# Kernel optimization log

Hardware: AMD Instinct MI355X
Metric: run time of the kernel (lower is better)

## Reference

```python
import jax, jax.numpy as jnp
import numpy as np

B, L, D, H, FF = 2, 4096, 512, 8, 2048
HD = D // H
EPS = 1e-5


def _layer_norm(x, g, b):
    mu = jnp.mean(x, axis=-1, keepdims=True)
    var = jnp.mean(jnp.square(x - mu), axis=-1, keepdims=True)
    return (x - mu) * jax.lax.rsqrt(var + EPS) * g + b


def setup_inputs() -> dict:
    key = jax.random.key(0)
    ks = jax.random.split(key, 16)
    s = 1.0 / np.sqrt(D)
    inp = {
        'x': jax.random.normal(ks[0], (B, L, D), dtype=jnp.float32),
        'Wq': jax.random.normal(ks[1], (D, D), dtype=jnp.float32) * s,
        'bq': jnp.zeros((D,), jnp.float32),
        'Wk': jax.random.normal(ks[2], (D, D), dtype=jnp.float32) * s,
        'bk': jnp.zeros((D,), jnp.float32),
        'Wv': jax.random.normal(ks[3], (D, D), dtype=jnp.float32) * s,
        'bv': jnp.zeros((D,), jnp.float32),
        'Wo': jax.random.normal(ks[4], (D, D), dtype=jnp.float32) * s,
        'bo': jnp.zeros((D,), jnp.float32),
        'ln1_g': jnp.ones((D,), jnp.float32),
        'ln1_b': jnp.zeros((D,), jnp.float32),
        'W1': jax.random.normal(ks[5], (D, FF), dtype=jnp.float32) * s,
        'b1': jnp.zeros((FF,), jnp.float32),
        'W2': jax.random.normal(ks[6], (FF, D), dtype=jnp.float32) * (1.0 / np.sqrt(FF)),
        'b2': jnp.zeros((D,), jnp.float32),
        'ln2_g': jnp.ones((D,), jnp.float32),
        'ln2_b': jnp.zeros((D,), jnp.float32),
        'window': 128,
    }
    return inp


def reference(x, Wq, bq, Wk, bk, Wv, bv, Wo, bo, ln1_g, ln1_b, W1, b1, W2, b2, ln2_g, ln2_b, window):
    # ---- local (banded) self-attention, matching nn.MultiheadAttention math ----
    q = (x @ Wq + bq).reshape(B, L, H, HD)
    k = (x @ Wk + bk).reshape(B, L, H, HD)
    v = (x @ Wv + bv).reshape(B, L, H, HD)
    scale = 1.0 / np.sqrt(HD)
    scores = jnp.einsum('bqhd,bkhd->bhqk', q, k) * scale  # [B,H,L,L]
    idx = jnp.arange(L)
    band = jnp.abs(idx[None, :] - idx[:, None]) > window   # True = masked
    scores = jnp.where(band[None, None], -jnp.inf, scores)
    probs = jax.nn.softmax(scores, axis=-1)
    attn = jnp.einsum('bhqk,bkhd->bqhd', probs, v).reshape(B, L, D)
    attn = attn @ Wo + bo
    # ---- residual + norm1 ----
    h = _layer_norm(x + attn, ln1_g, ln1_b)
    # ---- FFN + residual + norm2 (dropout=0 at eval) ----
    ff = jax.nn.relu(h @ W1 + b1) @ W2 + b2
    return _layer_norm(h + ff, ln2_g, ln2_b)
```

## Files before the change

kernel.cpp:

```cpp
#include <hip/hip_runtime.h>

namespace {

constexpr int B = 2, L = 4096, D = 512, H = 8, FF = 2048;
constexpr int M = B * L;
constexpr float LN_EPS = 1e-5f;

typedef __attribute__((ext_vector_type(8))) short short8;
typedef __attribute__((ext_vector_type(4))) float floatx4;

typedef __attribute__((address_space(3))) unsigned int lds_uint;
typedef const __attribute__((address_space(1))) unsigned int glob_uint;

__device__ __forceinline__ void gl_lds16(const unsigned short* g, unsigned short* l) {
  __builtin_amdgcn_global_load_lds((glob_uint*)g, (lds_uint*)l, 16, 0, 0);
}

__device__ __forceinline__ unsigned short f2bf(float f) {
  union { float f; unsigned u; } v; v.f = f;
  unsigned r = v.u + 0x7FFFu + ((v.u >> 16) & 1u);
  return (unsigned short)(r >> 16);
}

__global__ void k_prep(const float* __restrict__ x,
                       const float* __restrict__ Wq, const float* __restrict__ Wk,
                       const float* __restrict__ Wv, const float* __restrict__ Wo,
                       const float* __restrict__ W1, const float* __restrict__ W2,
                       const float* __restrict__ bq, const float* __restrict__ bk,
                       const float* __restrict__ bv,
                       unsigned short* __restrict__ Xb,
                       unsigned short* __restrict__ WqkvT,
                       unsigned short* __restrict__ WoT,
                       unsigned short* __restrict__ W1T,
                       unsigned short* __restrict__ W2T,
                       float* __restrict__ bqkv) {
  int tid = blockIdx.x * blockDim.x + threadIdx.x;
  if (tid < 1048576) {
    float4 v = ((const float4*)x)[tid];
    ushort4 o = make_ushort4(f2bf(v.x), f2bf(v.y), f2bf(v.z), f2bf(v.w));
    ((ushort4*)Xb)[tid] = o;
    return;
  }
  int u = tid - 1048576;
  if (u < 786432) {
    const float* src = (u < 262144) ? Wq : (u < 524288 ? Wk : Wv);
    int uu = u & 262143;
    int n = uu >> 9, k = uu & 511;
    WqkvT[u] = f2bf(src[k * 512 + n]);
    return;
  }
  u -= 786432;
  if (u < 262144) { int n = u >> 9, k = u & 511; WoT[u] = f2bf(Wo[k * 512 + n]); return; }
  u -= 262144;
  if (u < 1048576) { int n = u >> 9, k = u & 511; W1T[u] = f2bf(W1[k * 2048 + n]); return; }
  u -= 1048576;
  if (u < 1048576) { int n = u >> 11, k = u & 2047; W2T[u] = f2bf(W2[k * 512 + n]); return; }
  u -= 1048576;
  if (u < 1536) bqkv[u] = (u < 512) ? bq[u] : (u < 1024 ? bk[u - 512] : bv[u - 1024]);
}

template <int EPI>
__global__ __launch_bounds__(256, 3)
void k_gemm(const unsigned short* __restrict__ A, const unsigned short* __restrict__ BT,
            const float* __restrict__ bias, void* __restrict__ Cout,
            const int klen, const int N) {
  __shared__ unsigned short lA[128 * 32];
  __shared__ unsigned short lB[128 * 32];
  const int tid = threadIdx.x;
  const int wave = tid >> 6, lane = tid & 63;
  const int quad = lane >> 4, l16 = lane & 15;
  const int m0 = blockIdx.y * 128, n0 = blockIdx.x * 128;
  const int wm = (wave >> 1) * 64, wn = (wave & 1) * 64;
  const int kbeg = blockIdx.z * klen;
  const size_t Kdim = (size_t)klen * gridDim.z;

  const floatx4 fzero = {0.f, 0.f, 0.f, 0.f};
  floatx4 acc[4][4];
#pragma unroll
  for (int i = 0; i < 4; ++i)
#pragma unroll
    for (int j = 0; j < 4; ++j) acc[i][j] = fzero;

  const int r0 = tid >> 2, o0 = (tid & 3) * 8;
  const int r1 = (256 + tid) >> 2, o1 = (tid & 3) * 8;
  const unsigned short* Ag0 = A + (size_t)(m0 + r0) * Kdim + kbeg + o0;
  const unsigned short* Ag1 = A + (size_t)(m0 + r1) * Kdim + kbeg + o1;
  const unsigned short* Bg0 = BT + (size_t)(n0 + r0) * Kdim + kbeg + o0;
  const unsigned short* Bg1 = BT + (size_t)(n0 + r1) * Kdim + kbeg + o1;
  unsigned short* lA0 = &lA[wave * 512];
  unsigned short* lA1 = &lA[(4 + wave) * 512];
  unsigned short* lB0 = &lB[wave * 512];
  unsigned short* lB1 = &lB[(4 + wave) * 512];

  for (int kt = 0; kt < klen; kt += 32) {
    __syncthreads();
    gl_lds16(Ag0 + kt, lA0);
    gl_lds16(Ag1 + kt, lA1);
    gl_lds16(Bg0 + kt, lB0);
    gl_lds16(Bg1 + kt, lB1);
    __syncthreads();
    short8 af[4], bf[4];
#pragma unroll
    for (int i = 0; i < 4; ++i) af[i] = *(const short8*)&lA[(wm + i * 16 + l16) * 32 + quad * 8];
#pragma unroll
    for (int j = 0; j < 4; ++j) bf[j] = *(const short8*)&lB[(wn + j * 16 + l16) * 32 + quad * 8];
#pragma unroll
    for (int i = 0; i < 4; ++i)
#pragma unroll
      for (int j = 0; j < 4; ++j)
        acc[i][j] = __builtin_amdgcn_mfma_f32_16x16x32_bf16(af[i], bf[j], acc[i][j], 0, 0, 0);
  }

  float* outf = (float*)Cout + (size_t)blockIdx.z * M * N;
#pragma unroll
  for (int j = 0; j < 4; ++j) {
    const int col = n0 + wn + j * 16 + l16;
    const float bv = (blockIdx.z == 0) ? bias[col] : 0.f;
#pragma unroll
    for (int i = 0; i < 4; ++i) {
      const int row = m0 + wm + i * 16 + quad * 4;
#pragma unroll
      for (int r = 0; r < 4; ++r) {
        float v = acc[i][j][r] + bv;
        if (EPI == 1) v = fmaxf(v, 0.f);
        if (EPI == 2)
          outf[(size_t)(row + r) * N + col] = v;
        else
          ((unsigned short*)Cout)[(size_t)(row + r) * N + col] = f2bf(v);
      }
    }
  }
}

__global__ __launch_bounds__(256, 3)
void k_attn(const unsigned short* __restrict__ QKV, unsigned short* __restrict__ attnb,
            const int* __restrict__ wptr) {
  const int W = wptr[0];
  constexpr int VS = 324;
  __shared__ unsigned short Vt[64 * VS];
  __shared__ unsigned short Pb[4][16 * 72];
  const int tid = threadIdx.x;
  const int wave = tid >> 6, lane = tid & 63;
  const int quad = lane >> 4, l16 = lane & 15;
  const int blk = blockIdx.x;
  const int h = blk & 7, b = (blk >> 3) & 1, qt = blk >> 4;
  const int q0blk = qt * 64;
  const int q0 = q0blk + wave * 16;
  const float scale = 0.125f;

  const unsigned short* Kbase = QKV + (size_t)(b * L) * 1536 + 512 + h * 64;
  const unsigned short* Vbase = QKV + (size_t)(b * L) * 1536 + 1024 + h * 64;

#pragma unroll
  for (int i = 0; i < 10; ++i) {
    int c = tid + i * 256;
    int row = c >> 3, cd = (c & 7) * 8;
    int key = q0blk - 128 + row;
    int keyc = key < 0 ? 0 : (key > L - 1 ? L - 1 : key);
    short8 v = *(const short8*)(Vbase + (size_t)keyc * 1536 + cd);
#pragma unroll
    for (int e = 0; e < 8; ++e) Vt[(cd + e) * VS + row] = (unsigned short)v[e];
  }

  const unsigned short* Qp = QKV + (size_t)(b * L + q0 + l16) * 1536 + h * 64;
  short8 qf0 = *(const short8*)(Qp + quad * 8);
  short8 qf1 = *(const short8*)(Qp + 32 + quad * 8);

  const floatx4 fzero = {0.f, 0.f, 0.f, 0.f};
  floatx4 o[4];
#pragma unroll
  for (int i = 0; i < 4; ++i) o[i] = fzero;
  float lsum[4] = {0.f, 0.f, 0.f, 0.f};
  unsigned short* lp = Pb[wave];

  __syncthreads();

  for (int it = 0; it < 5; ++it) {
    const int jbg = q0blk - 128 + it * 64;
    floatx4 s[4];
#pragma unroll
    for (int ct = 0; ct < 4; ++ct) {
      int key = jbg + ct * 16 + l16;
      int keyc = key < 0 ? 0 : (key > L - 1 ? L - 1 : key);
      const unsigned short* Kr = Kbase + (size_t)keyc * 1536;
      floatx4 z = fzero;
      z = __builtin_amdgcn_mfma_f32_16x16x32_bf16(qf0, *(const short8*)(Kr + quad * 8), z, 0, 0, 0);
      z = __builtin_amdgcn_mfma_f32_16x16x32_bf16(qf1, *(const short8*)(Kr + 32 + quad * 8), z, 0, 0, 0);
      s[ct] = z;
    }
#pragma unroll
    for (int r = 0; r < 4; ++r) {
      int q = q0 + quad * 4 + r;
#pragma unroll
      for (int ct = 0; ct < 4; ++ct) {
        int key = jbg + ct * 16 + l16;
        int d = q - key; d = d < 0 ? -d : d;
        bool ok = (key >= 0) && (key < L) && (d <= W);
        float p = ok ? __expf(s[ct][r] * scale) : 0.f;
        lsum[r] += p;
        lp[(quad * 4 + r) * 72 + ct * 16 + l16] = f2bf(p);
      }
    }
    short8 pf0 = *(const short8*)&lp[l16 * 72 + quad * 8];
    short8 pf1 = *(const short8*)&lp[l16 * 72 + 32 + quad * 8];
#pragma unroll
    for (int nt = 0; nt < 4; ++nt) {
      const unsigned short* vp = &Vt[(nt * 16 + l16) * VS + it * 64 + quad * 8];
      o[nt] = __builtin_amdgcn_mfma_f32_16x16x32_bf16(pf0, *(const short8*)vp, o[nt], 0, 0, 0);
      o[nt] = __builtin_amdgcn_mfma_f32_16x16x32_bf16(pf1, *(const short8*)(vp + 32), o[nt], 0, 0, 0);
    }
  }
#pragma unroll
  for (int r = 0; r < 4; ++r) {
#pragma unroll
    for (int dd = 1; dd < 16; dd <<= 1) lsum[r] += __shfl_xor(lsum[r], dd, 64);
  }
#pragma unroll
  for (int r = 0; r < 4; ++r) {
    float inv = 1.f / lsum[r];
    size_t base = (size_t)(b * L + q0 + quad * 4 + r) * 512 + h * 64;
#pragma unroll
    for (int nt = 0; nt < 4; ++nt)
      attnb[base + nt * 16 + l16] = f2bf(o[nt][r] * inv);
  }
}

template <int NP>
__global__ __launch_bounds__(256, 2)
void k_res_ln(const float* __restrict__ t0, const float* __restrict__ t1,
              const float* __restrict__ res,
              const float* __restrict__ gamma, const float* __restrict__ beta,
              float* __restrict__ outf, unsigned short* __restrict__ outb) {
  const int wave = threadIdx.x >> 6, lane = threadIdx.x & 63;
  const int row = blockIdx.x * 4 + wave;
  const float4* tv = (const float4*)(t0 + (size_t)row * D);
  const float4* rv = (const float4*)(res + (size_t)row * D);
  float4 a0 = tv[lane], a1 = tv[lane + 64];
  float4 b0 = rv[lane], b1 = rv[lane + 64];
  float4 y0 = make_float4(a0.x + b0.x, a0.y + b0.y, a0.z + b0.z, a0.w + b0.w);
  float4 y1 = make_float4(a1.x + b1.x, a1.y + b1.y, a1.z + b1.z, a1.w + b1.w);
  if (NP == 2) {
    const float4* uv = (const float4*)(t1 + (size_t)row * D);
    float4 c0 = uv[lane], c1 = uv[lane + 64];
    y0.x += c0.x; y0.y += c0.y; y0.z += c0.z; y0.w += c0.w;
    y1.x += c1.x; y1.y += c1.y; y1.z += c1.z; y1.w += c1.w;
  }
  float s = y0.x + y0.y + y0.z + y0.w + y1.x + y1.y + y1.z + y1.w;
  float q = y0.x * y0.x + y0.y * y0.y + y0.z * y0.z + y0.w * y0.w +
            y1.x * y1.x + y1.y * y1.y + y1.z * y1.z + y1.w * y1.w;
#pragma unroll
  for (int d = 1; d < 64; d <<= 1) {
    s += __shfl_xor(s, d, 64);
    q += __shfl_xor(q, d, 64);
  }
  const float mean = s * (1.f / D);
  const float var = q * (1.f / D) - mean * mean;
  const float rstd = rsqrtf(var + LN_EPS);
  float4 g0 = ((const float4*)gamma)[lane], g1 = ((const float4*)gamma)[lane + 64];
  float4 e0 = ((const float4*)beta)[lane], e1 = ((const float4*)beta)[lane + 64];
  float4 o0 = make_float4((y0.x - mean) * rstd * g0.x + e0.x, (y0.y - mean) * rstd * g0.y + e0.y,
                          (y0.z - mean) * rstd * g0.z + e0.z, (y0.w - mean) * rstd * g0.w + e0.w);
  float4 o1 = make_float4((y1.x - mean) * rstd * g1.x + e1.x, (y1.y - mean) * rstd * g1.y + e1.y,
                          (y1.z - mean) * rstd * g1.z + e1.z, (y1.w - mean) * rstd * g1.w + e1.w);
  ((float4*)(outf + (size_t)row * D))[lane] = o0;
  ((float4*)(outf + (size_t)row * D))[lane + 64] = o1;
  if (outb) {
    ((ushort4*)(outb + (size_t)row * D))[lane] =
        make_ushort4(f2bf(o0.x), f2bf(o0.y), f2bf(o0.z), f2bf(o0.w));
    ((ushort4*)(outb + (size_t)row * D))[lane + 64] =
        make_ushort4(f2bf(o1.x), f2bf(o1.y), f2bf(o1.z), f2bf(o1.w));
  }
}

}

extern "C" void kernel_launch(void* const* d_in, const int* in_sizes, int n_in,
                              void* d_out, int out_size, void* d_ws, size_t ws_size,
                              hipStream_t stream) {
  const float* x   = (const float*)d_in[0];
  const float* Wq  = (const float*)d_in[1];
  const float* bq  = (const float*)d_in[2];
  const float* Wk  = (const float*)d_in[3];
  const float* bk  = (const float*)d_in[4];
  const float* Wv  = (const float*)d_in[5];
  const float* bv  = (const float*)d_in[6];
  const float* Wo  = (const float*)d_in[7];
  const float* bo  = (const float*)d_in[8];
  const float* g1  = (const float*)d_in[9];
  const float* be1 = (const float*)d_in[10];
  const float* W1  = (const float*)d_in[11];
  const float* b1  = (const float*)d_in[12];
  const float* W2  = (const float*)d_in[13];
  const float* b2  = (const float*)d_in[14];
  const float* g2  = (const float*)d_in[15];
  const float* be2 = (const float*)d_in[16];
  const int* wptr  = (const int*)d_in[17];
  float* out = (float*)d_out;

  char* w = (char*)d_ws;
  size_t off = 0;
  auto take = [&](size_t bytes) -> void* {
    void* p = w + off;
    off += (bytes + 255) & ~(size_t)255;
    return p;
  };
  unsigned short* Xb    = (unsigned short*)take((size_t)M * D * 2);
  unsigned short* QKVb  = (unsigned short*)take((size_t)M * 1536 * 2);
  unsigned short* attnb = (unsigned short*)take((size_t)M * D * 2);
  unsigned short* WqkvT = (unsigned short*)take((size_t)1536 * 512 * 2);
  unsigned short* WoT   = (unsigned short*)take((size_t)512 * 512 * 2);
  unsigned short* W1T   = (unsigned short*)take((size_t)2048 * 512 * 2);
  unsigned short* W2T   = (unsigned short*)take((size_t)512 * 2048 * 2);
  float* bqkv           = (float*)take(1536 * 4);
  float* tbuf           = (float*)take((size_t)2 * M * D * 4);
  float* hbuf           = (float*)take((size_t)M * D * 4);
  unsigned short* hb    = (unsigned short*)take((size_t)M * D * 2);
  unsigned short* ffb   = (unsigned short*)take((size_t)M * FF * 2);

  k_prep<<<16390, 256, 0, stream>>>(x, Wq, Wk, Wv, Wo, W1, W2, bq, bk, bv,
                                    Xb, WqkvT, WoT, W1T, W2T, bqkv);
  k_gemm<0><<<dim3(12, 64, 1), 256, 0, stream>>>(Xb, WqkvT, bqkv, QKVb, 512, 1536);
  k_attn<<<B * H * (L / 64), 256, 0, stream>>>(QKVb, attnb, wptr);
  k_gemm<2><<<dim3(4, 64, 2), 256, 0, stream>>>(attnb, WoT, bo, tbuf, 256, 512);
  k_res_ln<2><<<M / 4, 256, 0, stream>>>(tbuf, tbuf + (size_t)M * D, x, g1, be1, hbuf, hb);
  k_gemm<1><<<dim3(16, 64, 1), 256, 0, stream>>>(hb, W1T, b1, ffb, 512, 2048);
  k_gemm<2><<<dim3(4, 64, 2), 256, 0, stream>>>(ffb, W2T, b2, tbuf, 1024, 512);
  k_res_ln<2><<<M / 4, 256, 0, stream>>>(tbuf, tbuf + (size_t)M * D, hbuf, g2, be2, out, nullptr);
}
```

Before: 270.6 us.

## Tile weight transposes through LDS, swizzle attention V tile, reorder attention blocks

```diff
diff --git a/kernel.cpp b/kernel.cpp
--- a/kernel.cpp
+++ b/kernel.cpp
@@ -23,40 +23,64 @@
 }
 
 __global__ void k_prep(const float* __restrict__ x,
-                       const float* __restrict__ Wq, const float* __restrict__ Wk,
-                       const float* __restrict__ Wv, const float* __restrict__ Wo,
-                       const float* __restrict__ W1, const float* __restrict__ W2,
                        const float* __restrict__ bq, const float* __restrict__ bk,
                        const float* __restrict__ bv,
-                       unsigned short* __restrict__ Xb,
-                       unsigned short* __restrict__ WqkvT,
-                       unsigned short* __restrict__ WoT,
-                       unsigned short* __restrict__ W1T,
-                       unsigned short* __restrict__ W2T,
-                       float* __restrict__ bqkv) {
+                       unsigned short* __restrict__ Xb, float* __restrict__ bqkv) {
   int tid = blockIdx.x * blockDim.x + threadIdx.x;
   if (tid < 1048576) {
     float4 v = ((const float4*)x)[tid];
-    ushort4 o = make_ushort4(f2bf(v.x), f2bf(v.y), f2bf(v.z), f2bf(v.w));
-    ((ushort4*)Xb)[tid] = o;
+    ((ushort4*)Xb)[tid] = make_ushort4(f2bf(v.x), f2bf(v.y), f2bf(v.z), f2bf(v.w));
     return;
   }
   int u = tid - 1048576;
-  if (u < 786432) {
-    const float* src = (u < 262144) ? Wq : (u < 524288 ? Wk : Wv);
-    int uu = u & 262143;
-    int n = uu >> 9, k = uu & 511;
-    WqkvT[u] = f2bf(src[k * 512 + n]);
-    return;
-  }
-  u -= 786432;
-  if (u < 262144) { int n = u >> 9, k = u & 511; WoT[u] = f2bf(Wo[k * 512 + n]); return; }
-  u -= 262144;
-  if (u < 1048576) { int n = u >> 9, k = u & 511; W1T[u] = f2bf(W1[k * 2048 + n]); return; }
-  u -= 1048576;
-  if (u < 1048576) { int n = u >> 11, k = u & 2047; W2T[u] = f2bf(W2[k * 512 + n]); return; }
-  u -= 1048576;
   if (u < 1536) bqkv[u] = (u < 512) ? bq[u] : (u < 1024 ? bk[u - 512] : bv[u - 1024]);
+}
+
+__global__ __launch_bounds__(256)
+void k_tr(const float* __restrict__ Wq, const float* __restrict__ Wk,
+          const float* __restrict__ Wv, const float* __restrict__ Wo,
+          const float* __restrict__ W1, const float* __restrict__ W2,
+          unsigned short* __restrict__ WqkvT, unsigned short* __restrict__ WoT,
+          unsigned short* __restrict__ W1T, unsigned short* __restrict__ W2T) {
+  __shared__ unsigned short tile[64 * 72];
+  const int t = blockIdx.x;
+  const float* src; unsigned short* dst; int Ns, Kd, n0, k0, nsrc0;
+  if (t < 192) {
+    int nt = t % 24, kt = t / 24; int ng = nt * 64;
+    src = ng < 512 ? Wq : (ng < 1024 ? Wk : Wv);
+    Ns = 512; Kd = 512; n0 = ng; nsrc0 = ng & 511; k0 = kt * 64; dst = WqkvT;
+  } else if (t < 256) {
+    int u = t - 192; int nt = u % 8, kt = u / 8;
+    src = Wo; Ns = 512; Kd = 512; n0 = nt * 64; nsrc0 = n0; k0 = kt * 64; dst = WoT;
+  } else if (t < 512) {
+    int u = t - 256; int nt = u % 32, kt = u / 32;
+    src = W1; Ns = 2048; Kd = 512; n0 = nt * 64; nsrc0 = n0; k0 = kt * 64; dst = W1T;
+  } else {
+    int u = t - 512; int nt = u % 8, kt = u / 8;
+    src = W2; Ns = 512; Kd = 2048; n0 = nt * 64; nsrc0 = n0; k0 = kt * 64; dst = W2T;
+  }
+  const int tid = threadIdx.x;
+  {
+    int r = tid >> 2, cs = (tid & 3) * 16;
+    const float4* sp = (const float4*)(src + (size_t)(k0 + r) * Ns + nsrc0 + cs);
+    unsigned short* tp = &tile[r * 72 + cs];
+#pragma unroll
+    for (int i = 0; i < 4; ++i) {
+      float4 v = sp[i];
+      tp[i * 4 + 0] = f2bf(v.x); tp[i * 4 + 1] = f2bf(v.y);
+      tp[i * 4 + 2] = f2bf(v.z); tp[i * 4 + 3] = f2bf(v.w);
+    }
+  }
+  __syncthreads();
+  {
+    int n = tid >> 2, ks = (tid & 3) * 16;
+    unsigned short buf[16];
+#pragma unroll
+    for (int e = 0; e < 16; ++e) buf[e] = tile[(ks + e) * 72 + n];
+    unsigned short* dp = dst + (size_t)(n0 + n) * Kd + k0 + ks;
+    *(short8*)dp = *(const short8*)&buf[0];
+    *(short8*)(dp + 8) = *(const short8*)&buf[8];
+  }
 }
 
 template <int EPI>
@@ -143,7 +167,7 @@
   const int wave = tid >> 6, lane = tid & 63;
   const int quad = lane >> 4, l16 = lane & 15;
   const int blk = blockIdx.x;
-  const int h = blk & 7, b = (blk >> 3) & 1, qt = blk >> 4;
+  const int qt = blk & 63, h = (blk >> 6) & 7, b = blk >> 9;
   const int q0blk = qt * 64;
   const int q0 = q0blk + wave * 16;
   const float scale = 0.125f;
@@ -158,8 +182,9 @@
     int key = q0blk - 128 + row;
     int keyc = key < 0 ? 0 : (key > L - 1 ? L - 1 : key);
     short8 v = *(const short8*)(Vbase + (size_t)keyc * 1536 + cd);
-#pragma unroll
-    for (int e = 0; e < 8; ++e) Vt[(cd + e) * VS + row] = (unsigned short)v[e];
+    int rs = row ^ cd;
+#pragma unroll
+    for (int e = 0; e < 8; ++e) Vt[(cd + e) * VS + rs] = (unsigned short)v[e];
   }
 
   const unsigned short* Qp = QKV + (size_t)(b * L + q0 + l16) * 1536 + h * 64;
@@ -205,9 +230,11 @@
     short8 pf1 = *(const short8*)&lp[l16 * 72 + 32 + quad * 8];
 #pragma unroll
     for (int nt = 0; nt < 4; ++nt) {
-      const unsigned short* vp = &Vt[(nt * 16 + l16) * VS + it * 64 + quad * 8];
-      o[nt] = __builtin_amdgcn_mfma_f32_16x16x32_bf16(pf0, *(const short8*)vp, o[nt], 0, 0, 0);
-      o[nt] = __builtin_amdgcn_mfma_f32_16x16x32_bf16(pf1, *(const short8*)(vp + 32), o[nt], 0, 0, 0);
+      const int k8r = ((nt * 2 + (l16 >> 3)) & 7) * 8;
+      const unsigned short* vp0 = &Vt[(nt * 16 + l16) * VS + ((it * 64 + quad * 8) ^ k8r)];
+      const unsigned short* vp1 = &Vt[(nt * 16 + l16) * VS + ((it * 64 + 32 + quad * 8) ^ k8r)];
+      o[nt] = __builtin_amdgcn_mfma_f32_16x16x32_bf16(pf0, *(const short8*)vp0, o[nt], 0, 0, 0);
+      o[nt] = __builtin_amdgcn_mfma_f32_16x16x32_bf16(pf1, *(const short8*)vp1, o[nt], 0, 0, 0);
     }
   }
 #pragma unroll
@@ -317,8 +344,8 @@
   unsigned short* hb    = (unsigned short*)take((size_t)M * D * 2);
   unsigned short* ffb   = (unsigned short*)take((size_t)M * FF * 2);
 
-  k_prep<<<16390, 256, 0, stream>>>(x, Wq, Wk, Wv, Wo, W1, W2, bq, bk, bv,
-                                    Xb, WqkvT, WoT, W1T, W2T, bqkv);
+  k_prep<<<4102, 256, 0, stream>>>(x, bq, bk, bv, Xb, bqkv);
+  k_tr<<<768, 256, 0, stream>>>(Wq, Wk, Wv, Wo, W1, W2, WqkvT, WoT, W1T, W2T);
   k_gemm<0><<<dim3(12, 64, 1), 256, 0, stream>>>(Xb, WqkvT, bqkv, QKVb, 512, 1536);
   k_attn<<<B * H * (L / 64), 256, 0, stream>>>(QKVb, attnb, wptr);
   k_gemm<2><<<dim3(4, 64, 2), 256, 0, stream>>>(attnb, WoT, bo, tbuf, 256, 512);
```

Measured after the change: 265.9 us. About the same (-1.7%).
